# Kernel optimization log

Hardware: AMD Instinct MI355X
Metric: run time of the kernel (lower is better)

The kernel has to match this reference:

```python
import jax, jax.numpy as jnp
import numpy as np

B, S, D, F = 8, 2048, 256, 8

def setup_inputs() -> dict:
    key = jax.random.key(0)
    ks = jax.random.split(key, 7)
    hidden_states = jax.random.normal(ks[0], (B, S, D), dtype=jnp.float32)
    # flat indices into zero-prepended [1 + B*S, D] token table; 0 = padding row
    select_idx = jax.random.randint(ks[1], (B, S, F), 0, B * S + 1, dtype=jnp.int32)
    word_mask = jax.random.randint(ks[2], (B, S), 0, 2, dtype=jnp.int32)
    W1 = jax.random.normal(ks[3], (D, D), dtype=jnp.float32) * (1.0 / np.sqrt(D))
    b1 = jax.random.normal(ks[4], (D,), dtype=jnp.float32) * 0.02
    w2 = jax.random.normal(ks[5], (D,), dtype=jnp.float32) * (1.0 / np.sqrt(D))
    b2 = jax.random.normal(ks[6], (1,), dtype=jnp.float32) * 0.02
    return {"hidden_states": hidden_states, "select_idx": select_idx,
            "word_mask": word_mask, "W1": W1, "b1": b1, "w2": w2, "b2": b2}

def reference(hidden_states, select_idx, word_mask, W1, b1, w2, b2):
    b, s, d = hidden_states.shape
    h = jnp.tanh(hidden_states.reshape(-1, d) @ W1.T + b1)          # [B*S, D]
    h = jnp.concatenate([jnp.zeros((1, d), h.dtype), h], axis=0)    # zero padding row at index 0
    g = h[select_idx.reshape(-1)]                                    # gather: [B*S*F, D]
    g = g.reshape(b * s, -1, d).max(axis=1)                          # AdaptiveMaxPool1d(1) over word occurrences
    scores = (g @ w2 + b2[0]).reshape(b, s)                          # w2 linear -> [B, S]
    neg = -10000.0 * (1.0 - word_mask.astype(jnp.float32))
    return scores.astype(jnp.float32) + neg
```

## Files before the change

kernel.cpp:

```cpp
#include <hip/hip_runtime.h>
#include <hip/hip_bf16.h>
#include <math.h>

#define BB 8
#define SS 2048
#define DD 256
#define FF 8
#define NTOK (BB*SS)

typedef __bf16 bf16x8 __attribute__((ext_vector_type(8)));
typedef float  f32x4  __attribute__((ext_vector_type(4)));
typedef float  f32x2  __attribute__((ext_vector_type(2)));

#define BM 32

__device__ __forceinline__ unsigned pack2_bf16(float a, float b) {
    return (__float_as_uint(a) >> 16) | (__float_as_uint(b) & 0xFFFF0000u);
}
__device__ __forceinline__ float fast_tanh(float x) {
    float e = __expf(2.0f * x);
    return 1.0f - 2.0f * __builtin_amdgcn_rcpf(e + 1.0f);
}
__device__ __forceinline__ unsigned char f32_to_fp8(float v) {
    return (unsigned char)(__builtin_amdgcn_cvt_pk_fp8_f32(v, v, 0, false) & 0xFF);
}
__device__ __forceinline__ bf16x8 pack_bf16x8(f32x4 a, f32x4 b) {
    uint4 p;
    p.x = pack2_bf16(a.x, a.y); p.y = pack2_bf16(a.z, a.w);
    p.z = pack2_bf16(b.x, b.y); p.w = pack2_bf16(b.z, b.w);
    return *(bf16x8*)&p;
}

__global__ __launch_bounds__(512, 4) void gemm_tanh_kernel(
    const float* __restrict__ x, const float* __restrict__ W1,
    const float* __restrict__ b1, unsigned char* __restrict__ table)
{
    __shared__ __align__(16) unsigned short xs[BM * DD];

    const int tid  = threadIdx.x;
    const int bx   = blockIdx.x;
    const int tok0 = bx * BM;

    if (bx == 0 && tid < 64) ((unsigned int*)table)[tid] = 0u;

    const int wave = tid >> 6, lane = tid & 63;
    const int n0 = wave * 32;
    const int lr = lane & 15;
    const int kg = lane >> 4;
    const int sw = lr & 7;

    #pragma unroll
    for (int p = 0; p < 4; ++p) {
        int s = p * 512 + tid;
        int row = s >> 6, k4 = s & 63;
        f32x4 v = *(const f32x4*)&x[(size_t)(tok0 + row) * DD + k4 * 4];
        uint2 pk;
        pk.x = pack2_bf16(v.x, v.y);
        pk.y = pack2_bf16(v.z, v.w);
        int g  = k4 >> 1;
        int gp = g ^ (row & 7);
        *(uint2*)&xs[row * DD + gp * 8 + (k4 & 1) * 4] = pk;
    }
    __syncthreads();

    f32x4 acc[2][2];
    #pragma unroll
    for (int mf = 0; mf < 2; ++mf)
        #pragma unroll
        for (int nf = 0; nf < 2; ++nf)
            acc[mf][nf] = (f32x4){0.f, 0.f, 0.f, 0.f};

    const float* wrowf0 = W1 + (size_t)(n0 + lr) * DD + kg * 8;
    const float* wrowf1 = W1 + (size_t)(n0 + 16 + lr) * DD + kg * 8;

    #pragma unroll
    for (int c = 0; c < 8; ++c) {
        int gp8 = ((c * 4 + kg) ^ sw) * 8;
        bf16x8 af0 = *(const bf16x8*)&xs[lr * DD + gp8];
        bf16x8 af1 = *(const bf16x8*)&xs[(16 + lr) * DD + gp8];
        f32x4 w0a = *(const f32x4*)&wrowf0[c * 32];
        f32x4 w0b = *(const f32x4*)&wrowf0[c * 32 + 4];
        f32x4 w1a = *(const f32x4*)&wrowf1[c * 32];
        f32x4 w1b = *(const f32x4*)&wrowf1[c * 32 + 4];
        bf16x8 bf0 = pack_bf16x8(w0a, w0b);
        bf16x8 bf1 = pack_bf16x8(w1a, w1b);
        acc[0][0] = __builtin_amdgcn_mfma_f32_16x16x32_bf16(af0, bf0, acc[0][0], 0, 0, 0);
        acc[0][1] = __builtin_amdgcn_mfma_f32_16x16x32_bf16(af0, bf1, acc[0][1], 0, 0, 0);
        acc[1][0] = __builtin_amdgcn_mfma_f32_16x16x32_bf16(af1, bf0, acc[1][0], 0, 0, 0);
        acc[1][1] = __builtin_amdgcn_mfma_f32_16x16x32_bf16(af1, bf1, acc[1][1], 0, 0, 0);
    }

    float bj0 = b1[n0 + lr];
    float bj1 = b1[n0 + 16 + lr];

    __syncthreads();
    unsigned char* sc = (unsigned char*)&xs[0];
    #pragma unroll
    for (int mf = 0; mf < 2; ++mf) {
        #pragma unroll
        for (int nf = 0; nf < 2; ++nf) {
            #pragma unroll
            for (int r = 0; r < 4; ++r) {
                int row = mf * 16 + kg * 4 + r;
                int col = n0 + nf * 16 + lr;
                float v = fast_tanh(acc[mf][nf][r] + (nf ? bj1 : bj0));
                sc[row * 272 + col] = f32_to_fp8(v);
            }
        }
    }
    __syncthreads();
    {
        int row = tid >> 4;
        int off = (tid & 15) * 16;
        uint4 v = *(const uint4*)&sc[row * 272 + off];
        *(uint4*)&table[(size_t)(1 + tok0 + row) * DD + off] = v;
    }
}

__global__ __launch_bounds__(256) void gather_score_kernel(
    const unsigned char* __restrict__ table,
    const int* __restrict__ select_idx,
    const int* __restrict__ word_mask,
    const float* __restrict__ w2,
    const float* __restrict__ b2,
    float* __restrict__ out)
{
    const int tid  = threadIdx.x;
    const int lane = tid & 63;
    const int wv   = tid >> 6;
    const int i    = blockIdx.x * 4 + wv;
    const int half = lane >> 5;
    const int c    = lane & 31;
    const int d0   = c * 8;

    const int4* sp = (const int4*)(select_idx + (size_t)i * FF);
    int4 q0 = sp[0], q1 = sp[1];
    int rows[4];
    rows[0] = half ? q0.y : q0.x;
    rows[1] = half ? q0.w : q0.z;
    rows[2] = half ? q1.y : q1.x;
    rows[3] = half ? q1.w : q1.z;

    float m[8];
    #pragma unroll
    for (int j = 0; j < 8; ++j) m[j] = -INFINITY;

    #pragma unroll
    for (int it = 0; it < 4; ++it) {
        uint2 u = *(const uint2*)(table + (size_t)rows[it] * DD + d0);
        f32x2 a0 = __builtin_amdgcn_cvt_pk_f32_fp8(u.x, false);
        f32x2 a1 = __builtin_amdgcn_cvt_pk_f32_fp8(u.x, true);
        f32x2 a2 = __builtin_amdgcn_cvt_pk_f32_fp8(u.y, false);
        f32x2 a3 = __builtin_amdgcn_cvt_pk_f32_fp8(u.y, true);
        m[0] = fmaxf(m[0], a0.x); m[1] = fmaxf(m[1], a0.y);
        m[2] = fmaxf(m[2], a1.x); m[3] = fmaxf(m[3], a1.y);
        m[4] = fmaxf(m[4], a2.x); m[5] = fmaxf(m[5], a2.y);
        m[6] = fmaxf(m[6], a3.x); m[7] = fmaxf(m[7], a3.y);
    }

    #pragma unroll
    for (int j = 0; j < 8; ++j) m[j] = fmaxf(m[j], __shfl_xor(m[j], 32));

    f32x4 wa = *(const f32x4*)&w2[d0];
    f32x4 wb = *(const f32x4*)&w2[d0 + 4];
    float p = m[0] * wa.x + m[1] * wa.y + m[2] * wa.z + m[3] * wa.w
            + m[4] * wb.x + m[5] * wb.y + m[6] * wb.z + m[7] * wb.w;

    #pragma unroll
    for (int off = 16; off; off >>= 1) p += __shfl_xor(p, off);

    if (lane == 0) {
        float neg = word_mask[i] ? 0.f : -10000.f;
        out[i] = p + b2[0] + neg;
    }
}

extern "C" void kernel_launch(void* const* d_in, const int* in_sizes, int n_in,
                              void* d_out, int out_size, void* d_ws, size_t ws_size,
                              hipStream_t stream) {
    const float* hs    = (const float*)d_in[0];
    const int*   sidx  = (const int*)  d_in[1];
    const int*   wmask = (const int*)  d_in[2];
    const float* W1    = (const float*)d_in[3];
    const float* b1    = (const float*)d_in[4];
    const float* w2    = (const float*)d_in[5];
    const float* b2    = (const float*)d_in[6];
    float* out = (float*)d_out;

    unsigned char* table = (unsigned char*)d_ws;

    gemm_tanh_kernel<<<NTOK / BM, 512, 0, stream>>>(hs, W1, b1, table);
    gather_score_kernel<<<NTOK / 4, 256, 0, stream>>>(table, sidx, wmask, w2, b2, out);
}
```

Measured before the change: 97.17 us.

## Stage W1 chunks through LDS as bf16 with register-prefetched double buffering

The GEMM kernel no longer has each wave read its W1 rows straight from global memory and convert them per MFMA. It now loads 64-row chunks of W1 cooperatively, converts them to bf16 into a swizzled shared buffer, and prefetches the next chunk into registers while the MFMAs run. The wave-to-tile mapping also changes, so each wave owns one 16-row M fragment and one 16-col N slice per chunk. This cuts redundant global W1 reads and conversion work per wave, at the cost of extra LDS (32KB more per block, which lowers occupancy), extra barriers, and more registers for the prefetch.

```diff
diff --git a/kernel.cpp b/kernel.cpp
--- a/kernel.cpp
+++ b/kernel.cpp
@@ -13,6 +13,8 @@
 typedef float  f32x2  __attribute__((ext_vector_type(2)));
 
 #define BM 32
+#define WCH 64
+#define NCH (DD/WCH)
 
 __device__ __forceinline__ unsigned pack2_bf16(float a, float b) {
     return (__float_as_uint(a) >> 16) | (__float_as_uint(b) & 0xFFFF0000u);
@@ -23,12 +25,6 @@
 }
 __device__ __forceinline__ unsigned char f32_to_fp8(float v) {
     return (unsigned char)(__builtin_amdgcn_cvt_pk_fp8_f32(v, v, 0, false) & 0xFF);
-}
-__device__ __forceinline__ bf16x8 pack_bf16x8(f32x4 a, f32x4 b) {
-    uint4 p;
-    p.x = pack2_bf16(a.x, a.y); p.y = pack2_bf16(a.z, a.w);
-    p.z = pack2_bf16(b.x, b.y); p.w = pack2_bf16(b.z, b.w);
-    return *(bf16x8*)&p;
 }
 
 __global__ __launch_bounds__(512, 4) void gemm_tanh_kernel(
@@ -36,6 +32,7 @@
     const float* __restrict__ b1, unsigned char* __restrict__ table)
 {
     __shared__ __align__(16) unsigned short xs[BM * DD];
+    __shared__ __align__(16) unsigned short wb[WCH * DD];
 
     const int tid  = threadIdx.x;
     const int bx   = blockIdx.x;
@@ -44,10 +41,35 @@
     if (bx == 0 && tid < 64) ((unsigned int*)table)[tid] = 0u;
 
     const int wave = tid >> 6, lane = tid & 63;
-    const int n0 = wave * 32;
+    const int mf = wave >> 2;
+    const int nf = wave & 3;
     const int lr = lane & 15;
     const int kg = lane >> 4;
     const int sw = lr & 7;
+
+    f32x4 wr[8];
+    auto wload = [&](int nc) {
+        #pragma unroll
+        for (int p = 0; p < 8; ++p) {
+            int s = p * 512 + tid;
+            int row = s >> 6, k4 = s & 63;
+            wr[p] = *(const f32x4*)&W1[(size_t)(nc * WCH + row) * DD + k4 * 4];
+        }
+    };
+    auto wstore = [&]() {
+        #pragma unroll
+        for (int p = 0; p < 8; ++p) {
+            int s = p * 512 + tid;
+            int row = s >> 6, k4 = s & 63;
+            uint2 pk;
+            pk.x = pack2_bf16(wr[p].x, wr[p].y);
+            pk.y = pack2_bf16(wr[p].z, wr[p].w);
+            int gp = (k4 >> 1) ^ (row & 7);
+            *(uint2*)&wb[row * DD + gp * 8 + (k4 & 1) * 4] = pk;
+        }
+    };
+
+    wload(0);
 
     #pragma unroll
     for (int p = 0; p < 4; ++p) {
@@ -57,55 +79,51 @@
         uint2 pk;
         pk.x = pack2_bf16(v.x, v.y);
         pk.y = pack2_bf16(v.z, v.w);
-        int g  = k4 >> 1;
-        int gp = g ^ (row & 7);
+        int gp = (k4 >> 1) ^ (row & 7);
         *(uint2*)&xs[row * DD + gp * 8 + (k4 & 1) * 4] = pk;
     }
+
+    wstore();
     __syncthreads();
 
-    f32x4 acc[2][2];
-    #pragma unroll
-    for (int mf = 0; mf < 2; ++mf)
-        #pragma unroll
-        for (int nf = 0; nf < 2; ++nf)
-            acc[mf][nf] = (f32x4){0.f, 0.f, 0.f, 0.f};
-
-    const float* wrowf0 = W1 + (size_t)(n0 + lr) * DD + kg * 8;
-    const float* wrowf1 = W1 + (size_t)(n0 + 16 + lr) * DD + kg * 8;
-
-    #pragma unroll
-    for (int c = 0; c < 8; ++c) {
-        int gp8 = ((c * 4 + kg) ^ sw) * 8;
-        bf16x8 af0 = *(const bf16x8*)&xs[lr * DD + gp8];
-        bf16x8 af1 = *(const bf16x8*)&xs[(16 + lr) * DD + gp8];
-        f32x4 w0a = *(const f32x4*)&wrowf0[c * 32];
-        f32x4 w0b = *(const f32x4*)&wrowf0[c * 32 + 4];
-        f32x4 w1a = *(const f32x4*)&wrowf1[c * 32];
-        f32x4 w1b = *(const f32x4*)&wrowf1[c * 32 + 4];
-        bf16x8 bf0 = pack_bf16x8(w0a, w0b);
-        bf16x8 bf1 = pack_bf16x8(w1a, w1b);
-        acc[0][0] = __builtin_amdgcn_mfma_f32_16x16x32_bf16(af0, bf0, acc[0][0], 0, 0, 0);
-        acc[0][1] = __builtin_amdgcn_mfma_f32_16x16x32_bf16(af0, bf1, acc[0][1], 0, 0, 0);
-        acc[1][0] = __builtin_amdgcn_mfma_f32_16x16x32_bf16(af1, bf0, acc[1][0], 0, 0, 0);
-        acc[1][1] = __builtin_amdgcn_mfma_f32_16x16x32_bf16(af1, bf1, acc[1][1], 0, 0, 0);
-    }
-
-    float bj0 = b1[n0 + lr];
-    float bj1 = b1[n0 + 16 + lr];
-
-    __syncthreads();
+    f32x4 acc[NCH];
+    #pragma unroll
+    for (int nc = 0; nc < NCH; ++nc) acc[nc] = (f32x4){0.f, 0.f, 0.f, 0.f};
+
+    const int arow = mf * 16 + lr;
+    const int nrow = nf * 16 + lr;
+
+    #pragma unroll
+    for (int nc = 0; nc < NCH; ++nc) {
+        if (nc + 1 < NCH) wload(nc + 1);
+
+        #pragma unroll
+        for (int c = 0; c < 8; ++c) {
+            int gp8 = ((c * 4 + kg) ^ sw) * 8;
+            bf16x8 af = *(const bf16x8*)&xs[arow * DD + gp8];
+            bf16x8 bf = *(const bf16x8*)&wb[nrow * DD + gp8];
+            acc[nc] = __builtin_amdgcn_mfma_f32_16x16x32_bf16(af, bf, acc[nc], 0, 0, 0);
+        }
+        __syncthreads();
+        if (nc + 1 < NCH) {
+            wstore();
+            __syncthreads();
+        }
+    }
+
+    float bj[NCH];
+    #pragma unroll
+    for (int nc = 0; nc < NCH; ++nc) bj[nc] = b1[nc * WCH + nf * 16 + lr];
+
     unsigned char* sc = (unsigned char*)&xs[0];
     #pragma unroll
-    for (int mf = 0; mf < 2; ++mf) {
-        #pragma unroll
-        for (int nf = 0; nf < 2; ++nf) {
-            #pragma unroll
-            for (int r = 0; r < 4; ++r) {
-                int row = mf * 16 + kg * 4 + r;
-                int col = n0 + nf * 16 + lr;
-                float v = fast_tanh(acc[mf][nf][r] + (nf ? bj1 : bj0));
-                sc[row * 272 + col] = f32_to_fp8(v);
-            }
+    for (int nc = 0; nc < NCH; ++nc) {
+        #pragma unroll
+        for (int r = 0; r < 4; ++r) {
+            int row = mf * 16 + kg * 4 + r;
+            int col = nc * WCH + nf * 16 + lr;
+            float v = fast_tanh(acc[nc][r] + bj[nc]);
+            sc[row * 272 + col] = f32_to_fp8(v);
         }
     }
     __syncthreads();
```

Measured after the change: 90.51 us. 6.8% less time.
